# Kernel optimization log

Hardware: AMD Instinct MI355X
Metric: run time of the kernel (lower is better)

The kernel has to match this reference:

```python
import jax, jax.numpy as jnp
import numpy as np

EPS = 1e-5

def _conv(x, w, b, groups=1, pad=0):
    # x: NCHW, w: OIHW (I = in_ch/groups)
    y = jax.lax.conv_general_dilated(
        x, w, window_strides=(1, 1), padding=[(pad, pad), (pad, pad)],
        feature_group_count=groups,
        dimension_numbers=('NCHW', 'OIHW', 'NCHW'))
    return y + b[None, :, None, None]

def _bn(x, g, b, m, v):
    scale = g * jax.lax.rsqrt(v + EPS)
    return x * scale[None, :, None, None] + (b - m * scale)[None, :, None, None]

def _block(x, w_dw, b_dw, w_pw, b_pw, g, b, m, v, groups):
    h = _conv(x, w_dw, b_dw, groups=groups, pad=1)   # 3x3 grouped conv
    h = _conv(h, w_pw, b_pw)                          # 1x1 pointwise 2C->C
    return jax.nn.relu(_bn(h, g, b, m, v))

def setup_inputs() -> dict:
    key = jax.random.key(0)
    ks = jax.random.split(key, 16)
    B, C, H, W = 4, 256, 64, 64
    s = 0.02  # small weight scale to keep softmax logits well-conditioned
    return {
        'x1': jax.random.normal(ks[0], (B, C, H, W), jnp.float32),
        'x2': jax.random.normal(ks[1], (B, C, H, W), jnp.float32),
        'w1_dw': jax.random.normal(ks[2], (2 * C, 2, 3, 3), jnp.float32) * s,
        'b1_dw': jnp.zeros((2 * C,), jnp.float32),
        'w1_pw': jax.random.normal(ks[3], (C, 2 * C, 1, 1), jnp.float32) * s,
        'b1_pw': jnp.zeros((C,), jnp.float32),
        'bn1_g': jnp.ones((C,), jnp.float32),
        'bn1_b': jnp.zeros((C,), jnp.float32),
        'bn1_m': jnp.zeros((C,), jnp.float32),
        'bn1_v': jnp.ones((C,), jnp.float32),
        'w2_dw': jax.random.normal(ks[4], (2 * C, 2, 3, 3), jnp.float32) * s,
        'b2_dw': jnp.zeros((2 * C,), jnp.float32),
        'w2_pw': jax.random.normal(ks[5], (C, 2 * C, 1, 1), jnp.float32) * s,
        'b2_pw': jnp.zeros((C,), jnp.float32),
        'bn2_g': jnp.ones((C,), jnp.float32),
        'bn2_b': jnp.zeros((C,), jnp.float32),
        'bn2_m': jnp.zeros((C,), jnp.float32),
        'bn2_v': jnp.ones((C,), jnp.float32),
        'wq': jax.random.normal(ks[6], (C // 8, C, 1, 1), jnp.float32) * s,
        'bq': jnp.zeros((C // 8,), jnp.float32),
        'wk': jax.random.normal(ks[7], (C // 8, C, 1, 1), jnp.float32) * s,
        'bk': jnp.zeros((C // 8,), jnp.float32),
        'wv': jax.random.normal(ks[8], (C, C, 1, 1), jnp.float32) * s,
        'bv': jnp.zeros((C,), jnp.float32),
        'gamma': jnp.ones((1,), jnp.float32),
    }

def reference(x1, x2,
              w1_dw, b1_dw, w1_pw, b1_pw, bn1_g, bn1_b, bn1_m, bn1_v,
              w2_dw, b2_dw, w2_pw, b2_pw, bn2_g, bn2_b, bn2_m, bn2_v,
              wq, bq, wk, bk, wv, bv, gamma):
    B, C, H, W = x1.shape
    N = H * W
    sub = x1 - x2
    concat1 = jnp.concatenate([sub, x1], axis=1)  # [B,2C,H,W]
    concat2 = jnp.concatenate([sub, x2], axis=1)
    x3 = _block(concat1, w1_dw, b1_dw, w1_pw, b1_pw, bn1_g, bn1_b, bn1_m, bn1_v, groups=C)
    x4 = _block(concat2, w2_dw, b2_dw, w2_pw, b2_pw, bn2_g, bn2_b, bn2_m, bn2_v, groups=C)
    q = _conv(x4, wq, bq).reshape(B, -1, N)   # [B, C//8, N]
    k = _conv(x3, wk, bk).reshape(B, -1, N)   # [B, C//8, N]
    v = _conv(x3, wv, bv).reshape(B, C, N)    # [B, C, N]
    energy = jnp.einsum('bdq,bdk->bqk', q, k)          # [B, N, N]
    attn = jax.nn.softmax(energy, axis=-1)
    out = jnp.einsum('bck,bqk->bcq', v, attn)          # [B, C, N]
    out = out.reshape(B, C, H, W)
    return gamma[0] * out + x1
```

## Files before the change

kernel.cpp:

```cpp
#include <hip/hip_runtime.h>
#include <hip/hip_bf16.h>

#define EPSB 1e-5f

typedef __hip_bfloat16 bf16;
typedef __attribute__((ext_vector_type(8))) short bf16x8;
typedef __attribute__((ext_vector_type(4))) float f32x4;

__device__ __forceinline__ unsigned short f2bu(float x) {
  bf16 h = __float2bfloat16(x);
  return *reinterpret_cast<unsigned short*>(&h);
}
__device__ __forceinline__ unsigned int pk2(float lo, float hi) {
  return ((unsigned int)f2bu(hi) << 16) | (unsigned int)f2bu(lo);
}

__global__ __launch_bounds__(256) void k_dwconv3(
    const float* __restrict__ x1, const float* __restrict__ x2,
    const float* __restrict__ w1, const float* __restrict__ b1,
    const float* __restrict__ w2, const float* __restrict__ b2,
    const float* __restrict__ w1pw, const float* __restrict__ w2pw,
    bf16* __restrict__ h1, bf16* __restrict__ h2,
    bf16* __restrict__ o1, bf16* __restrict__ o2) {
  if (blockIdx.y == 4) {
    int x = blockIdx.x;
    if (x < 128) {
      int i = (x * 256 + threadIdx.x) * 4;
      float4 a = *(const float4*)(w1pw + i);
      float4 c = *(const float4*)(w2pw + i);
      uint2 ua = {pk2(a.x, a.y), pk2(a.z, a.w)};
      uint2 uc = {pk2(c.x, c.y), pk2(c.z, c.w)};
      *(uint2*)&o1[i] = ua;
      *(uint2*)&o2[i] = uc;
    }
    return;
  }

  __shared__ float img[2 * 64 * 64];
  int g = blockIdx.x, b = blockIdx.y;
  int t = threadIdx.x;
  int row = t >> 2, x0 = (t & 3) * 16;
  bool xlo = (x0 == 0), xhi = (x0 == 48);
  size_t obase = (((size_t)(b * 512 + 2 * g)) << 12) + row * 64 + x0;

  auto stencil = [&](const float* wp, float bs0, float bs1, bf16* hout) {
    float o0[16], o1v[16];
#pragma unroll
    for (int i = 0; i < 16; i++) { o0[i] = bs0; o1v[i] = bs1; }
#pragma unroll
    for (int ch = 0; ch < 2; ch++) {
      float wa[9], wb[9];
#pragma unroll
      for (int i = 0; i < 9; i++) { wa[i] = wp[ch * 9 + i]; wb[i] = wp[18 + ch * 9 + i]; }
      const float* ib = img + ch * 4096;
#pragma unroll
      for (int ky = 0; ky < 3; ky++) {
        int yy = row + ky - 1;
        if (yy < 0 || yy > 63) continue;
        const float* rp = ib + yy * 64 + x0;
        float4 q0 = *(const float4*)(rp);
        float4 q1 = *(const float4*)(rp + 4);
        float4 q2 = *(const float4*)(rp + 8);
        float4 q3 = *(const float4*)(rp + 12);
        float v[18];
        v[0] = xlo ? 0.f : rp[-1];
        v[1] = q0.x;  v[2] = q0.y;  v[3] = q0.z;  v[4] = q0.w;
        v[5] = q1.x;  v[6] = q1.y;  v[7] = q1.z;  v[8] = q1.w;
        v[9] = q2.x;  v[10] = q2.y; v[11] = q2.z; v[12] = q2.w;
        v[13] = q3.x; v[14] = q3.y; v[15] = q3.z; v[16] = q3.w;
        v[17] = xhi ? 0.f : rp[16];
        float a0 = wa[ky * 3], a1 = wa[ky * 3 + 1], a2 = wa[ky * 3 + 2];
        float c0 = wb[ky * 3], c1 = wb[ky * 3 + 1], c2 = wb[ky * 3 + 2];
#pragma unroll
        for (int i = 0; i < 16; i++) {
          o0[i] += a0 * v[i] + a1 * v[i + 1] + a2 * v[i + 2];
          o1v[i] += c0 * v[i] + c1 * v[i + 1] + c2 * v[i + 2];
        }
      }
    }
    uint4 u0 = {pk2(o0[0], o0[1]), pk2(o0[2], o0[3]), pk2(o0[4], o0[5]), pk2(o0[6], o0[7])};
    uint4 u1 = {pk2(o0[8], o0[9]), pk2(o0[10], o0[11]), pk2(o0[12], o0[13]), pk2(o0[14], o0[15])};
    *(uint4*)&hout[obase] = u0;
    *(uint4*)&hout[obase + 8] = u1;
    uint4 w0 = {pk2(o1v[0], o1v[1]), pk2(o1v[2], o1v[3]), pk2(o1v[4], o1v[5]), pk2(o1v[6], o1v[7])};
    uint4 w1v = {pk2(o1v[8], o1v[9]), pk2(o1v[10], o1v[11]), pk2(o1v[12], o1v[13]), pk2(o1v[14], o1v[15])};
    *(uint4*)&hout[obase + 4096] = w0;
    *(uint4*)&hout[obase + 4096 + 8] = w1v;
  };

  if (g < 128) {
    const float4* p1 = (const float4*)(x1 + ((size_t)(b * 256 + 2 * g) << 12));
    const float4* p2 = (const float4*)(x2 + ((size_t)(b * 256 + 2 * g) << 12));
#pragma unroll
    for (int u = 0; u < 8; u++) {
      int i = u * 256 + t;
      float4 a = p1[i], c = p2[i];
      float4 d = {a.x - c.x, a.y - c.y, a.z - c.z, a.w - c.w};
      ((float4*)img)[i] = d;
    }
  } else {
    const float4* p1 = (const float4*)(x1 + ((size_t)(b * 256 + 2 * (g - 128)) << 12));
#pragma unroll
    for (int u = 0; u < 8; u++) {
      int i = u * 256 + t;
      ((float4*)img)[i] = p1[i];
    }
  }
  __syncthreads();
  stencil(w1 + (size_t)(2 * g) * 18, b1[2 * g], b1[2 * g + 1], h1);

  if (g >= 128) {
    __syncthreads();
    const float4* p2 = (const float4*)(x2 + ((size_t)(b * 256 + 2 * (g - 128)) << 12));
#pragma unroll
    for (int u = 0; u < 8; u++) {
      int i = u * 256 + t;
      ((float4*)img)[i] = p2[i];
    }
    __syncthreads();
  }
  stencil(w2 + (size_t)(2 * g) * 18, b2[2 * g], b2[2 * g + 1], h2);
}

__global__ __launch_bounds__(256) void k_gemm_pw2(
    const bf16* __restrict__ In1, const bf16* __restrict__ In2,
    const bf16* __restrict__ W1, const bf16* __restrict__ W2,
    const float* __restrict__ bias1, const float* __restrict__ bias2,
    const float* __restrict__ g1v, const float* __restrict__ be1,
    const float* __restrict__ m1v, const float* __restrict__ v1v,
    const float* __restrict__ g2v, const float* __restrict__ be2,
    const float* __restrict__ m2v, const float* __restrict__ v2v,
    bf16* __restrict__ Out1, bf16* __restrict__ Out2) {
  __shared__ __align__(16) bf16 Al[128][72];
  __shared__ __align__(16) bf16 Bl[128][72];

  int lin = (blockIdx.z * 2 + blockIdx.y) * 32 + blockIdx.x;
  int xcd = lin & 7, slot = lin >> 3;
  int sel = xcd >> 2, b = xcd & 3;
  int p0 = (slot & 31) * 128;
  int oc0 = (slot >> 5) * 128;

  const bf16* In    = sel ? In2 : In1;
  const bf16* W     = sel ? W2 : W1;
  const float* bias = sel ? bias2 : bias1;
  const float* bng  = sel ? g2v : g1v;
  const float* bnb  = sel ? be2 : be1;
  const float* bnm  = sel ? m2v : m1v;
  const float* bnv  = sel ? v2v : v1v;
  bf16* Out         = sel ? Out2 : Out1;

  int t = threadIdx.x;
  int w = t >> 6, lane = t & 63, l16 = lane & 15, quad = lane >> 4;
  int wr = w >> 1, wc = w & 1;
  const bf16* Inb = In + (size_t)b * 512 * 4096;

  f32x4 acc[4][4];
#pragma unroll
  for (int mi = 0; mi < 4; mi++)
#pragma unroll
    for (int nj = 0; nj < 4; nj++) acc[mi][nj] = (f32x4){0.f, 0.f, 0.f, 0.f};

  int ocl = t >> 1, kb = (t & 1) * 32;
  int sch = t >> 2, soct = sch >> 3, swi = sch & 7, spg4 = t & 3;

  for (int kc = 0; kc < 512; kc += 64) {
    __syncthreads();
    {
      const bf16* src = W + (size_t)(oc0 + ocl) * 512 + kc + kb;
      uint4 u0 = *(const uint4*)(src);
      uint4 u1 = *(const uint4*)(src + 8);
      uint4 u2 = *(const uint4*)(src + 16);
      uint4 u3 = *(const uint4*)(src + 24);
      *(uint4*)&Al[ocl][kb] = u0;
      *(uint4*)&Al[ocl][kb + 8] = u1;
      *(uint4*)&Al[ocl][kb + 16] = u2;
      *(uint4*)&Al[ocl][kb + 24] = u3;
    }
    {
      const bf16* src = Inb + (size_t)(kc + sch) * 4096 + p0 + spg4 * 32;
#pragma unroll
      for (int u = 0; u < 4; u++) {
        uint4 qv = *(const uint4*)(src + u * 8);
        const unsigned short* qs = (const unsigned short*)&qv;
        int pixb = spg4 * 32 + u * 8;
        int col = (((soct ^ (pixb >> 3)) & 7) << 3) | swi;
#pragma unroll
        for (int j = 0; j < 8; j++)
          *(unsigned short*)&Bl[pixb + j][col] = qs[j];
      }
    }
    __syncthreads();
#pragma unroll
    for (int h = 0; h < 2; h++) {
      bf16x8 af[4], bv[4];
#pragma unroll
      for (int mi = 0; mi < 4; mi++)
        af[mi] = *(const bf16x8*)&Al[wr * 64 + mi * 16 + l16][h * 32 + quad * 8];
#pragma unroll
      for (int nj = 0; nj < 4; nj++) {
        int s = (nj * 2 + (l16 >> 3)) & 7;
        bv[nj] = *(const bf16x8*)&Bl[wc * 64 + nj * 16 + l16][(((h * 4 + quad) ^ s) & 7) * 8];
      }
#pragma unroll
      for (int mi = 0; mi < 4; mi++)
#pragma unroll
        for (int nj = 0; nj < 4; nj++)
          acc[mi][nj] = __builtin_amdgcn_mfma_f32_16x16x32_bf16(
              af[mi], bv[nj], acc[mi][nj], 0, 0, 0);
    }
  }

#pragma unroll
  for (int mi = 0; mi < 4; mi++) {
    int ocb = oc0 + wr * 64 + mi * 16 + quad * 4;
    float4 bs4 = *(const float4*)&bias[ocb];
    float4 g4 = *(const float4*)&bng[ocb];
    float4 b4 = *(const float4*)&bnb[ocb];
    float4 m4 = *(const float4*)&bnm[ocb];
    float4 v4 = *(const float4*)&bnv[ocb];
    float sc[4], sh[4];
    sc[0] = g4.x * rsqrtf(v4.x + EPSB); sh[0] = bs4.x * sc[0] + b4.x - m4.x * sc[0];
    sc[1] = g4.y * rsqrtf(v4.y + EPSB); sh[1] = bs4.y * sc[1] + b4.y - m4.y * sc[1];
    sc[2] = g4.z * rsqrtf(v4.z + EPSB); sh[2] = bs4.z * sc[2] + b4.z - m4.z * sc[2];
    sc[3] = g4.w * rsqrtf(v4.w + EPSB); sh[3] = bs4.w * sc[3] + b4.w - m4.w * sc[3];
#pragma unroll
    for (int nj = 0; nj < 4; nj++) {
      int p = p0 + wc * 64 + nj * 16 + l16;
#pragma unroll
      for (int r = 0; r < 4; r++) {
        float val = fmaxf(acc[mi][nj][r] * sc[r] + sh[r], 0.f);
        Out[(((size_t)(b * 256 + ocb + r)) << 12) + p] = __float2bfloat16(val);
      }
    }
  }
}

__global__ __launch_bounds__(256) void k_gemm_qkv(
    const bf16* __restrict__ x3, const bf16* __restrict__ x4,
    const float* __restrict__ wv, const float* __restrict__ bv,
    const float* __restrict__ wq, const float* __restrict__ wk,
    const float* __restrict__ bq, const float* __restrict__ bk,
    bf16* __restrict__ vvb, bf16* __restrict__ qbf, bf16* __restrict__ kbf) {
  __shared__ __align__(16) bf16 Al[128][72];
  __shared__ __align__(16) bf16 Bl[128][72];

  int lin = (blockIdx.z * 2 + blockIdx.y) * 64 + blockIdx.x;
  int xcd = lin & 7, slot = lin >> 3;
  int b = xcd >> 1;
  int idx = ((xcd & 1) * 64) + slot;
  int by = idx >> 6;
  int bx = idx & 63;

  int t = threadIdx.x;
  int w = t >> 6, lane = t & 63, l16 = lane & 15, quad = lane >> 4;

  if (bx < 32) {
    int wr = w >> 1, wc = w & 1;
    int p0 = bx * 128;
    int oc0 = by * 128;
    const bf16* Inb = x3 + (size_t)b * 256 * 4096;

    f32x4 acc[4][4];
#pragma unroll
    for (int mi = 0; mi < 4; mi++)
#pragma unroll
      for (int nj = 0; nj < 4; nj++) acc[mi][nj] = (f32x4){0.f, 0.f, 0.f, 0.f};

    int ocl = t >> 1, kb = (t & 1) * 32;
    int sch = t >> 2, soct = sch >> 3, swi = sch & 7, spg4 = t & 3;

    for (int kc = 0; kc < 256; kc += 64) {
      __syncthreads();
      {
        const float* src = wv + (size_t)(oc0 + ocl) * 256 + kc + kb;
#pragma unroll
        for (int u = 0; u < 4; u++) {
          float4 f0 = *(const float4*)(src + u * 8);
          float4 f1 = *(const float4*)(src + u * 8 + 4);
          uint4 uu = {pk2(f0.x, f0.y), pk2(f0.z, f0.w), pk2(f1.x, f1.y), pk2(f1.z, f1.w)};
          *(uint4*)&Al[ocl][kb + u * 8] = uu;
        }
      }
      {
        const bf16* src = Inb + (size_t)(kc + sch) * 4096 + p0 + spg4 * 32;
#pragma unroll
        for (int u = 0; u < 4; u++) {
          uint4 qv = *(const uint4*)(src + u * 8);
          const unsigned short* qs = (const unsigned short*)&qv;
          int pixb = spg4 * 32 + u * 8;
          int col = (((soct ^ (pixb >> 3)) & 7) << 3) | swi;
#pragma unroll
          for (int j = 0; j < 8; j++)
            *(unsigned short*)&Bl[pixb + j][col] = qs[j];
        }
      }
      __syncthreads();
#pragma unroll
      for (int h = 0; h < 2; h++) {
        bf16x8 af[4], bvv[4];
#pragma unroll
        for (int mi = 0; mi < 4; mi++)
          af[mi] = *(const bf16x8*)&Al[wr * 64 + mi * 16 + l16][h * 32 + quad * 8];
#pragma unroll
        for (int nj = 0; nj < 4; nj++) {
          int s = (nj * 2 + (l16 >> 3)) & 7;
          bvv[nj] = *(const bf16x8*)&Bl[wc * 64 + nj * 16 + l16][(((h * 4 + quad) ^ s) & 7) * 8];
        }
#pragma unroll
        for (int mi = 0; mi < 4; mi++)
#pragma unroll
          for (int nj = 0; nj < 4; nj++)
            acc[mi][nj] = __builtin_amdgcn_mfma_f32_16x16x32_bf16(
                af[mi], bvv[nj], acc[mi][nj], 0, 0, 0);
      }
    }

#pragma unroll
    for (int mi = 0; mi < 4; mi++) {
      int ocb = oc0 + wr * 64 + mi * 16 + quad * 4;
      float4 bs4 = *(const float4*)&bv[ocb];
      float sh[4] = {bs4.x, bs4.y, bs4.z, bs4.w};
#pragma unroll
      for (int nj = 0; nj < 4; nj++) {
        int p = p0 + wc * 64 + nj * 16 + l16;
#pragma unroll
        for (int r = 0; r < 4; r++) {
          float val = acc[mi][nj][r] + sh[r];
          vvb[(((size_t)(b * 256 + ocb + r)) << 12) + p] = __float2bfloat16(val);
        }
      }
    }
  } else {
    int p0 = (bx - 32) * 128;
    const bf16* In  = (by == 0) ? x4 : x3;
    const float* W  = (by == 0) ? wq : wk;
    const float* bi = (by == 0) ? bq : bk;
    bf16* Out       = (by == 0) ? qbf : kbf;
    const bf16* Inb = In + (size_t)b * 256 * 4096;

    f32x4 acc[2][2];
#pragma unroll
    for (int mi = 0; mi < 2; mi++)
#pragma unroll
      for (int nj = 0; nj < 2; nj++) acc[mi][nj] = (f32x4){0.f, 0.f, 0.f, 0.f};

    int aocl = t >> 3, akb = (t & 7) * 4;
    int sch = t >> 3, soct = sch >> 3, swi = sch & 7, spg = t & 7;

    for (int kc = 0; kc < 256; kc += 32) {
      __syncthreads();
      {
        const float* src = W + (size_t)aocl * 256 + kc + akb;
        float4 f0 = *(const float4*)(src);
        uint2 u = {pk2(f0.x, f0.y), pk2(f0.z, f0.w)};
        *(uint2*)&Al[aocl][akb] = u;
      }
      {
        const bf16* src = Inb + (size_t)(kc + sch) * 4096 + p0 + spg * 16;
        uint4 qv0 = *(const uint4*)src;
        uint4 qv1 = *(const uint4*)(src + 8);
        const unsigned short* qs0 = (const unsigned short*)&qv0;
        const unsigned short* qs1 = (const unsigned short*)&qv1;
#pragma unroll
        for (int j = 0; j < 8; j++) {
          int pix = spg * 16 + j;
          int col = (((soct ^ (pix >> 3)) & 3) << 3) | swi;
          *(unsigned short*)&Bl[pix][col] = qs0[j];
        }
#pragma unroll
        for (int j = 0; j < 8; j++) {
          int pix = spg * 16 + 8 + j;
          int col = (((soct ^ (pix >> 3)) & 3) << 3) | swi;
          *(unsigned short*)&Bl[pix][col] = qs1[j];
        }
      }
      __syncthreads();
      bf16x8 af[2], bvv[2];
#pragma unroll
      for (int mi = 0; mi < 2; mi++)
        af[mi] = *(const bf16x8*)&Al[mi * 16 + l16][quad * 8];
#pragma unroll
      for (int nj = 0; nj < 2; nj++) {
        int s = (nj * 2 + (l16 >> 3)) & 3;
        bvv[nj] = *(const bf16x8*)&Bl[w * 32 + nj * 16 + l16][(quad ^ s) * 8];
      }
#pragma unroll
      for (int mi = 0; mi < 2; mi++)
#pragma unroll
        for (int nj = 0; nj < 2; nj++)
          acc[mi][nj] = __builtin_amdgcn_mfma_f32_16x16x32_bf16(
              af[mi], bvv[nj], acc[mi][nj], 0, 0, 0);
    }

#pragma unroll
    for (int mi = 0; mi < 2; mi++) {
      int ocb = mi * 16 + quad * 4;
      float4 bs4 = *(const float4*)&bi[ocb];
      float bs[4] = {bs4.x, bs4.y, bs4.z, bs4.w};
#pragma unroll
      for (int nj = 0; nj < 2; nj++) {
        int p = p0 + w * 32 + nj * 16 + l16;
        float v0 = acc[mi][nj][0] + bs[0];
        float v1 = acc[mi][nj][1] + bs[1];
        float v2 = acc[mi][nj][2] + bs[2];
        float v3 = acc[mi][nj][3] + bs[3];
        uint2 u = {pk2(v0, v1), pk2(v2, v3)};
        *(uint2*)&Out[((size_t)(b * 4096) + p) * 32 + ocb] = u;
      }
    }
  }
}

__global__ __launch_bounds__(512, 4) void k_attn_mfma(
    const bf16* __restrict__ qb, const bf16* __restrict__ kb,
    const bf16* __restrict__ vb, const float* __restrict__ x1,
    const float* __restrict__ gamma, float* __restrict__ out) {
  __shared__ __align__(16) bf16 Pl[2][64 * 128];
  __shared__ float lsumw[8][64];

  int t = threadIdx.x;
  int w = t >> 6, lane = t & 63;
  int l16 = lane & 15, quad = lane >> 4;

  int lin = blockIdx.y * 128 + blockIdx.x;
  int xcd = lin & 7, slot = lin >> 3;
  int b = xcd >> 1;
  int chalf = xcd & 1;
  int q0 = slot * 64;

  const bf16* kbb = kb + (size_t)b * 4096 * 32;
  const bf16* vbb = vb + ((size_t)(b * 256 + chalf * 128)) * 4096;

  bf16x8 qf[4];
#pragma unroll
  for (int nj = 0; nj < 4; nj++)
    qf[nj] = *(const bf16x8*)(qb + ((size_t)(b * 4096 + q0 + nj * 16 + l16)) * 32 + quad * 8);

  f32x4 acc[4];
#pragma unroll
  for (int nj = 0; nj < 4; nj++) acc[nj] = (f32x4){0.f, 0.f, 0.f, 0.f};
  float lpart[4] = {0.f, 0.f, 0.f, 0.f};

  const bf16* kptr = kbb + ((size_t)(w * 16 + l16)) * 32 + quad * 8;
  const bf16* vptr = vbb + ((size_t)(w * 16 + l16)) * 4096 + quad * 8;

  int c16w = w * 2 + (quad >> 1);
  int off8 = (quad & 1) * 4;

  auto load_kv = [&](int j0, bf16x8& kf, bf16x8 vf[4]) {
    kf = *(const bf16x8*)(kptr + (size_t)j0 * 32);
#pragma unroll
    for (int kc = 0; kc < 4; kc++)
      vf[kc] = *(const bf16x8*)(vptr + j0 + kc * 32);
  };

  auto s_phase = [&](const bf16x8& kf, int pb) {
    bf16* P = Pl[pb];
    __builtin_amdgcn_s_setprio(1);
#pragma unroll
    for (int nj = 0; nj < 4; nj++) {
      f32x4 s = __builtin_amdgcn_mfma_f32_16x16x32_bf16(
          kf, qf[nj], (f32x4){0.f, 0.f, 0.f, 0.f}, 0, 0, 0);
      float p0f = __expf(s[0]);
      float p1f = __expf(s[1]);
      float p2f = __expf(s[2]);
      float p3f = __expf(s[3]);
      lpart[nj] += (p0f + p1f) + (p2f + p3f);
      int row = nj * 16 + l16;
      int c16 = c16w ^ (row & 15);
      uint2 u = {pk2(p0f, p1f), pk2(p2f, p3f)};
      *(uint2*)&P[row * 128 + c16 * 8 + off8] = u;
    }
    __builtin_amdgcn_s_setprio(0);
  };

  auto pv_phase = [&](const bf16x8 vf[4], int pb) {
    const bf16* P = Pl[pb];
#pragma unroll
    for (int kc = 0; kc < 4; kc++) {
      bf16x8 pf[4];
#pragma unroll
      for (int nj = 0; nj < 4; nj++) {
        int row = nj * 16 + l16;
        int c16 = (kc * 4 + quad) ^ (row & 15);
        pf[nj] = *(const bf16x8*)&P[row * 128 + c16 * 8];
      }
      __builtin_amdgcn_s_setprio(1);
#pragma unroll
      for (int nj = 0; nj < 4; nj++)
        acc[nj] = __builtin_amdgcn_mfma_f32_16x16x32_bf16(
            vf[kc], pf[nj], acc[nj], 0, 0, 0);
      __builtin_amdgcn_s_setprio(0);
    }
  };

  bf16x8 kfA, kfB, vfA[4], vfB[4];
  load_kv(0, kfA, vfA);
  s_phase(kfA, 0);

  for (int i = 0; i < 32; i += 2) {
    __syncthreads();
    if (i < 31) load_kv((i + 1) * 128, kfB, vfB);
    pv_phase(vfA, 0);
    if (i < 31) s_phase(kfB, 1);
    __syncthreads();
    if (i + 2 < 32) load_kv((i + 2) * 128, kfA, vfA);
    if (i + 1 < 32) pv_phase(vfB, 1);
    if (i + 2 < 32) s_phase(kfA, 0);
  }

#pragma unroll
  for (int nj = 0; nj < 4; nj++) {
    float v = lpart[nj];
    v += __shfl_xor(v, 16);
    v += __shfl_xor(v, 32);
    lpart[nj] = v;
  }
  if (lane < 16) {
#pragma unroll
    for (int nj = 0; nj < 4; nj++) lsumw[w][nj * 16 + lane] = lpart[nj];
  }
  __syncthreads();

  float gm = gamma[0];
#pragma unroll
  for (int nj = 0; nj < 4; nj++) {
    int ql = nj * 16 + l16;
    float ls = 0.f;
#pragma unroll
    for (int w8 = 0; w8 < 8; w8++) ls += lsumw[w8][ql];
    float gl = gm / ls;
    int cb = chalf * 128 + w * 16 + quad * 4;
#pragma unroll
    for (int r = 0; r < 4; r++) {
      size_t gidx = (((size_t)(b * 256 + cb + r)) << 12) + q0 + ql;
      out[gidx] = gl * acc[nj][r] + x1[gidx];
    }
  }
}

extern "C" void kernel_launch(void* const* d_in, const int* in_sizes, int n_in,
                              void* d_out, int out_size, void* d_ws, size_t ws_size,
                              hipStream_t stream) {
  const float* x1    = (const float*)d_in[0];
  const float* x2    = (const float*)d_in[1];
  const float* w1_dw = (const float*)d_in[2];
  const float* b1_dw = (const float*)d_in[3];
  const float* w1_pw = (const float*)d_in[4];
  const float* b1_pw = (const float*)d_in[5];
  const float* bn1_g = (const float*)d_in[6];
  const float* bn1_b = (const float*)d_in[7];
  const float* bn1_m = (const float*)d_in[8];
  const float* bn1_v = (const float*)d_in[9];
  const float* w2_dw = (const float*)d_in[10];
  const float* b2_dw = (const float*)d_in[11];
  const float* w2_pw = (const float*)d_in[12];
  const float* b2_pw = (const float*)d_in[13];
  const float* bn2_g = (const float*)d_in[14];
  const float* bn2_b = (const float*)d_in[15];
  const float* bn2_m = (const float*)d_in[16];
  const float* bn2_v = (const float*)d_in[17];
  const float* wq    = (const float*)d_in[18];
  const float* bq    = (const float*)d_in[19];
  const float* wk    = (const float*)d_in[20];
  const float* bk    = (const float*)d_in[21];
  const float* wv    = (const float*)d_in[22];
  const float* bv    = (const float*)d_in[23];
  const float* gamma = (const float*)d_in[24];

  bf16* wsb = (bf16*)d_ws;
  bf16* h1  = wsb;
  bf16* h2  = wsb + 8388608;
  bf16* x3  = wsb + 16777216;
  bf16* x4  = wsb + 20971520;
  bf16* qbf = wsb + 25165824;
  bf16* kbf = wsb + 25690112;
  bf16* vvb = wsb + 26214400;
  bf16* w1b = vvb;
  bf16* w2b = vvb + 131072;

  k_dwconv3<<<dim3(256, 5), 256, 0, stream>>>(x1, x2, w1_dw, b1_dw, w2_dw, b2_dw,
                                              w1_pw, w2_pw, h1, h2, w1b, w2b);
  k_gemm_pw2<<<dim3(32, 2, 8), 256, 0, stream>>>(h1, h2, w1b, w2b, b1_pw, b2_pw,
                                                 bn1_g, bn1_b, bn1_m, bn1_v,
                                                 bn2_g, bn2_b, bn2_m, bn2_v, x3, x4);
  k_gemm_qkv<<<dim3(64, 2, 4), 256, 0, stream>>>(x3, x4, wv, bv, wq, wk, bq, bk,
                                                 vvb, qbf, kbf);
  k_attn_mfma<<<dim3(128, 4), 512, 0, stream>>>(qbf, kbf, vvb, x1, gamma, (float*)d_out);
}
```

Measured before the change: 255.2 us.

## Double-buffer LDS tiles and prefetch next K chunk in pointwise GEMM

Converts the pointwise 1x1 conv GEMM main loop into a software pipeline. Shared memory now holds two buffers, the next K chunk's global loads are issued into registers before the MFMA work on the current buffer, and they are written to the other buffer afterward, so each iteration needs one barrier instead of two. The aim is to hide global memory latency behind the matrix math. The cost is doubled LDS use (about 73KB per block), which may lower occupancy, plus extra registers held across the compute.

```diff
diff --git a/kernel.cpp b/kernel.cpp
--- a/kernel.cpp
+++ b/kernel.cpp
@@ -131,8 +131,8 @@
     const float* __restrict__ g2v, const float* __restrict__ be2,
     const float* __restrict__ m2v, const float* __restrict__ v2v,
     bf16* __restrict__ Out1, bf16* __restrict__ Out2) {
-  __shared__ __align__(16) bf16 Al[128][72];
-  __shared__ __align__(16) bf16 Bl[128][72];
+  __shared__ __align__(16) bf16 Al[2][128][72];
+  __shared__ __align__(16) bf16 Bl[2][128][72];
 
   int lin = (blockIdx.z * 2 + blockIdx.y) * 32 + blockIdx.x;
   int xcd = lin & 7, slot = lin >> 3;
@@ -163,43 +163,58 @@
   int ocl = t >> 1, kb = (t & 1) * 32;
   int sch = t >> 2, soct = sch >> 3, swi = sch & 7, spg4 = t & 3;
 
-  for (int kc = 0; kc < 512; kc += 64) {
-    __syncthreads();
-    {
-      const bf16* src = W + (size_t)(oc0 + ocl) * 512 + kc + kb;
-      uint4 u0 = *(const uint4*)(src);
-      uint4 u1 = *(const uint4*)(src + 8);
-      uint4 u2 = *(const uint4*)(src + 16);
-      uint4 u3 = *(const uint4*)(src + 24);
-      *(uint4*)&Al[ocl][kb] = u0;
-      *(uint4*)&Al[ocl][kb + 8] = u1;
-      *(uint4*)&Al[ocl][kb + 16] = u2;
-      *(uint4*)&Al[ocl][kb + 24] = u3;
-    }
-    {
-      const bf16* src = Inb + (size_t)(kc + sch) * 4096 + p0 + spg4 * 32;
-#pragma unroll
-      for (int u = 0; u < 4; u++) {
-        uint4 qv = *(const uint4*)(src + u * 8);
-        const unsigned short* qs = (const unsigned short*)&qv;
-        int pixb = spg4 * 32 + u * 8;
-        int col = (((soct ^ (pixb >> 3)) & 7) << 3) | swi;
-#pragma unroll
-        for (int j = 0; j < 8; j++)
-          *(unsigned short*)&Bl[pixb + j][col] = qs[j];
-      }
-    }
-    __syncthreads();
+  uint4 wreg0, wreg1, wreg2, wreg3, ireg0, ireg1, ireg2, ireg3;
+
+  auto load_regs = [&](int kc) {
+    const bf16* srcW = W + (size_t)(oc0 + ocl) * 512 + kc + kb;
+    wreg0 = *(const uint4*)(srcW);
+    wreg1 = *(const uint4*)(srcW + 8);
+    wreg2 = *(const uint4*)(srcW + 16);
+    wreg3 = *(const uint4*)(srcW + 24);
+    const bf16* srcI = Inb + (size_t)(kc + sch) * 4096 + p0 + spg4 * 32;
+    ireg0 = *(const uint4*)(srcI);
+    ireg1 = *(const uint4*)(srcI + 8);
+    ireg2 = *(const uint4*)(srcI + 16);
+    ireg3 = *(const uint4*)(srcI + 24);
+  };
+
+  auto store_lds = [&](int pb) {
+    *(uint4*)&Al[pb][ocl][kb] = wreg0;
+    *(uint4*)&Al[pb][ocl][kb + 8] = wreg1;
+    *(uint4*)&Al[pb][ocl][kb + 16] = wreg2;
+    *(uint4*)&Al[pb][ocl][kb + 24] = wreg3;
+    const uint4 iregs[4] = {ireg0, ireg1, ireg2, ireg3};
+#pragma unroll
+    for (int u = 0; u < 4; u++) {
+      const unsigned short* qs = (const unsigned short*)&iregs[u];
+      int pixb = spg4 * 32 + u * 8;
+      int col = (((soct ^ (pixb >> 3)) & 7) << 3) | swi;
+#pragma unroll
+      for (int j = 0; j < 8; j++)
+        *(unsigned short*)&Bl[pb][pixb + j][col] = qs[j];
+    }
+  };
+
+  load_regs(0);
+  store_lds(0);
+  __syncthreads();
+
+  for (int tt = 0; tt < 8; tt++) {
+    int cur = tt & 1;
+    if (tt < 7) {
+      load_regs((tt + 1) * 64);
+      __builtin_amdgcn_sched_barrier(0);
+    }
 #pragma unroll
     for (int h = 0; h < 2; h++) {
       bf16x8 af[4], bv[4];
 #pragma unroll
       for (int mi = 0; mi < 4; mi++)
-        af[mi] = *(const bf16x8*)&Al[wr * 64 + mi * 16 + l16][h * 32 + quad * 8];
+        af[mi] = *(const bf16x8*)&Al[cur][wr * 64 + mi * 16 + l16][h * 32 + quad * 8];
 #pragma unroll
       for (int nj = 0; nj < 4; nj++) {
         int s = (nj * 2 + (l16 >> 3)) & 7;
-        bv[nj] = *(const bf16x8*)&Bl[wc * 64 + nj * 16 + l16][(((h * 4 + quad) ^ s) & 7) * 8];
+        bv[nj] = *(const bf16x8*)&Bl[cur][wc * 64 + nj * 16 + l16][(((h * 4 + quad) ^ s) & 7) * 8];
       }
 #pragma unroll
       for (int mi = 0; mi < 4; mi++)
@@ -208,6 +223,8 @@
           acc[mi][nj] = __builtin_amdgcn_mfma_f32_16x16x32_bf16(
               af[mi], bv[nj], acc[mi][nj], 0, 0, 0);
     }
+    if (tt < 7) store_lds(cur ^ 1);
+    __syncthreads();
   }
 
 #pragma unroll
```

Result: no change. 253.1 us, median of 2 (-0.8%).
